# Kernel tuning notes

Hardware: AMD Instinct MI355X
Metric: run time of the kernel (lower is better)

## Reference

```python
import jax, jax.numpy as jnp
import numpy as np

HID = 2048
NH = 16
HD = HID // NH  # 128
SEQ = 2048
BSZ = 2
NEG = -1e9


def setup_inputs() -> dict:
    key = jax.random.key(0)
    ks = jax.random.split(key, 9)
    s = 0.02
    hidden_states = jax.random.normal(ks[0], (BSZ, SEQ, HID), jnp.float32)
    # additive causal mask [1,1,S,S]
    causal = jnp.tril(jnp.ones((SEQ, SEQ), jnp.bool_))
    attention_mask = jnp.where(causal, 0.0, NEG).astype(jnp.float32)[None, None]
    Wq = jax.random.normal(ks[1], (HID, NH * HD), jnp.float32) * s
    bq = jax.random.normal(ks[2], (NH * HD,), jnp.float32) * s
    Wk = jax.random.normal(ks[3], (HID, NH * HD), jnp.float32) * s
    bk = jax.random.normal(ks[4], (NH * HD,), jnp.float32) * s
    Wv = jax.random.normal(ks[5], (HID, NH * HD), jnp.float32) * s
    bv = jax.random.normal(ks[6], (NH * HD,), jnp.float32) * s
    Wo = jax.random.normal(ks[7], (NH * HD, HID), jnp.float32) * s
    return {"hidden_states": hidden_states, "attention_mask": attention_mask,
            "Wq": Wq, "bq": bq, "Wk": Wk, "bk": bk, "Wv": Wv, "bv": bv, "Wo": Wo}


def reference(hidden_states, attention_mask, Wq, bq, Wk, bk, Wv, bv, Wo):
    b, s, _ = hidden_states.shape
    # projections -> [b, h, s, d]
    q = (hidden_states @ Wq + bq).reshape(b, s, NH, HD).transpose(0, 2, 1, 3)
    k = (hidden_states @ Wk + bk).reshape(b, s, NH, HD).transpose(0, 2, 1, 3)
    v = (hidden_states @ Wv + bv).reshape(b, s, NH, HD).transpose(0, 2, 1, 3)
    # eager attention, materializing [b,h,s,s] scores as in the original
    scores = jnp.einsum('bhqd,bhkd->bhqk', q, k) / jnp.sqrt(jnp.float32(HD))
    scores = scores + attention_mask
    probs = jax.nn.softmax(scores.astype(jnp.float32), axis=-1).astype(q.dtype)
    ctx = jnp.einsum('bhqk,bhkd->bhqd', probs, v)
    ctx = ctx.transpose(0, 2, 1, 3).reshape(b, s, NH * HD)
    return ctx @ Wo
```

## Files before the change

### kernel.cpp

```cpp
#include <hip/hip_runtime.h>

#define SEQ 2048
#define HIDDEN 2048
#define NHEAD 16
#define HDIM 128
#define BSZ 2

typedef __attribute__((ext_vector_type(8))) short bf16x8;
typedef __attribute__((ext_vector_type(4))) float f32x4;
typedef __attribute__((ext_vector_type(16))) float f32x16;
typedef unsigned short u16;
typedef unsigned int u32;

__device__ __forceinline__ u16 f2bf(float f) {
  union { float f; u32 u; } v; v.f = f;
  u32 r = v.u + 0x7FFF + ((v.u >> 16) & 1);
  return (u16)(r >> 16);
}

__device__ __forceinline__ void gload_lds16(const void* g, void* l) {
  __builtin_amdgcn_global_load_lds((const __attribute__((address_space(1))) u32*)g,
                                   (__attribute__((address_space(3))) u32*)l, 16, 0, 0);
}

__device__ __forceinline__ u32 pkbf(float lo, float hi_) {
  u32 r;
  asm("v_cvt_pk_bf16_f32 %0, %1, %2" : "=v"(r) : "v"(lo), "v"(hi_));
  return r;
}

__device__ __forceinline__ void pl32swap(u32& a, u32& b) {
  asm("v_permlane32_swap_b32 %0, %1" : "+v"(a), "+v"(b));
}

__global__ void conv_hs_kernel(const float4* __restrict__ in, uint4* __restrict__ out) {
  int i = blockIdx.x * 256 + threadIdx.x;
  float4 a = in[2 * i], b = in[2 * i + 1];
  uint4 o;
  o.x = (u32)f2bf(a.x) | ((u32)f2bf(a.y) << 16);
  o.y = (u32)f2bf(a.z) | ((u32)f2bf(a.w) << 16);
  o.z = (u32)f2bf(b.x) | ((u32)f2bf(b.y) << 16);
  o.w = (u32)f2bf(b.z) | ((u32)f2bf(b.w) << 16);
  out[i] = o;
}

__global__ void transw_kernel(const float* __restrict__ W0, const float* __restrict__ W1,
                              const float* __restrict__ W2, const float* __restrict__ W3,
                              u16* __restrict__ T0, u16* __restrict__ T1,
                              u16* __restrict__ T2, u16* __restrict__ T3) {
  __shared__ float tile[32][33];
  const float* W; u16* T;
  switch (blockIdx.z) {
    case 0: W = W0; T = T0; break;
    case 1: W = W1; T = T1; break;
    case 2: W = W2; T = T2; break;
    default: W = W3; T = T3; break;
  }
  int n0 = blockIdx.x * 32, k0 = blockIdx.y * 32;
  int tx = threadIdx.x, ty = threadIdx.y;
  #pragma unroll
  for (int r = ty; r < 32; r += 8) tile[r][tx] = W[(k0 + r) * HIDDEN + n0 + tx];
  __syncthreads();
  #pragma unroll
  for (int r = ty; r < 32; r += 8) T[(n0 + r) * HIDDEN + k0 + tx] = f2bf(tile[tx][r]);
}

__device__ __forceinline__ void stageA8(const u16* Ag, u16* Al, int kt, int h, int tid) {
  const int c = tid;
  const int row = h * 64 + (c >> 3);
  const int slot = (c & 7) ^ (row & 7);
  gload_lds16(Ag + (size_t)row * HIDDEN + kt * 64 + slot * 8,
              (char*)Al + h * 8192 + c * 16);
}
__device__ __forceinline__ void stageB8(const u16* Bg, u16* Bl, int kt, int h, int tid) {
  #pragma unroll
  for (int i = 0; i < 2; i++) {
    const int c = tid + i * 512;
    const int row = h * 128 + (c >> 3);
    const int slot = (c & 7) ^ (row & 7);
    gload_lds16(Bg + (size_t)row * HIDDEN + kt * 64 + slot * 8,
                (char*)Bl + h * 16384 + c * 16);
  }
}

#define LDA8(dst, QA, mi, ks) { \
  const int row_ = (QA) * 64 + wr * 32 + (mi) * 16 + l15; \
  dst = *(const bf16x8*)((const char*)Acur + row_ * 128 + ((((ks) * 4 + l4) ^ (row_ & 7)) * 16)); }
#define LDB8(dst, QB, ni, ks) { \
  const int row_ = (QB) * 128 + wc * 32 + (ni) * 16 + l15; \
  dst = *(const bf16x8*)((const char*)Bcur + row_ * 128 + ((((ks) * 4 + l4) ^ (row_ & 7)) * 16)); }

#define MFMA_(a, b, c) __builtin_amdgcn_mfma_f32_16x16x32_bf16(a, b, c, 0, 0, 0)

#define PHASE8(QA, QB, STG, VM) { \
  bf16x8 a00, a10, a01, a11, b00, b10, b01, b11; \
  LDA8(a00, QA, 0, 0) LDA8(a10, QA, 1, 0) LDA8(a01, QA, 0, 1) LDA8(a11, QA, 1, 1) \
  LDB8(b00, QB, 0, 0) LDB8(b10, QB, 1, 0) LDB8(b01, QB, 0, 1) LDB8(b11, QB, 1, 1) \
  STG; \
  __builtin_amdgcn_s_barrier(); \
  __builtin_amdgcn_s_setprio(1); \
  acc[QA][QB][0][0] = MFMA_(a00, b00, acc[QA][QB][0][0]); \
  acc[QA][QB][0][1] = MFMA_(a00, b10, acc[QA][QB][0][1]); \
  acc[QA][QB][1][0] = MFMA_(a10, b00, acc[QA][QB][1][0]); \
  acc[QA][QB][1][1] = MFMA_(a10, b10, acc[QA][QB][1][1]); \
  acc[QA][QB][0][0] = MFMA_(a01, b01, acc[QA][QB][0][0]); \
  acc[QA][QB][0][1] = MFMA_(a01, b11, acc[QA][QB][0][1]); \
  acc[QA][QB][1][0] = MFMA_(a11, b01, acc[QA][QB][1][0]); \
  acc[QA][QB][1][1] = MFMA_(a11, b11, acc[QA][QB][1][1]); \
  __builtin_amdgcn_s_setprio(0); \
  asm volatile("s_waitcnt vmcnt(" VM ")" ::: "memory"); \
  __builtin_amdgcn_sched_barrier(0); \
  __builtin_amdgcn_s_barrier(); }

#define GEMM8_CORE(Ag, Bg) \
  __shared__ u16 AL[2][128 * 64]; \
  __shared__ u16 BL[2][256 * 64]; \
  const int tid = threadIdx.x, lane = tid & 63, w = tid >> 6; \
  const int wr = w >> 2, wc = w & 3, l15 = lane & 15, l4 = (lane >> 4) & 3; \
  f32x4 acc[2][2][2][2] = {}; \
  stageA8(Ag, AL[0], 0, 0, tid); \
  __builtin_amdgcn_sched_barrier(0); \
  stageB8(Bg, BL[0], 0, 0, tid); \
  __builtin_amdgcn_sched_barrier(0); \
  stageB8(Bg, BL[0], 0, 1, tid); \
  __builtin_amdgcn_sched_barrier(0); \
  stageA8(Ag, AL[0], 0, 1, tid); \
  asm volatile("s_waitcnt vmcnt(3)" ::: "memory"); \
  __builtin_amdgcn_sched_barrier(0); \
  __builtin_amdgcn_s_barrier(); \
  for (int t = 0; t < HIDDEN / 64; t++) { \
    const int cb = t & 1; \
    const u16* Acur = AL[cb]; const u16* Bcur = BL[cb]; \
    u16* An = AL[cb ^ 1]; u16* Bn = BL[cb ^ 1]; \
    const int kn = (t < HIDDEN / 64 - 1) ? t + 1 : t;   \
    PHASE8(0, 0, stageA8(Ag, An, kn, 0, tid), "2") \
    PHASE8(0, 1, stageB8(Bg, Bn, kn, 0, tid), "3") \
    PHASE8(1, 0, stageB8(Bg, Bn, kn, 1, tid), "5") \
    PHASE8(1, 1, stageA8(Ag, An, kn, 1, tid), "3") \
  }

__global__ __launch_bounds__(512, 1)
void qkv_gemm8(const u16* __restrict__ hsb, const u16* __restrict__ wT,
               const float* __restrict__ bq, const float* __restrict__ bk,
               const float* __restrict__ bv,
               u16* __restrict__ Qb, u16* __restrict__ Kb, u16* __restrict__ Vb) {
  const int o = blockIdx.x;
  const int wg = (o & 7) * 96 + (o >> 3);
  const int by = wg / 24, bx = wg % 24;
  const int z = bx >> 3;
  const u16* Ag = hsb + (size_t)by * 128 * HIDDEN;
  const u16* Bg = wT + (size_t)bx * 256 * HIDDEN;
  u16* dst = (z == 0) ? Qb : (z == 1) ? Kb : Vb;
  const float* bias = (z == 0) ? bq : (z == 1) ? bk : bv;
  const float scale = (z == 0) ? 0.08838834764831845f * 1.4426950408889634f : 1.0f;

  GEMM8_CORE(Ag, Bg)

  #pragma unroll
  for (int qa = 0; qa < 2; qa++)
    #pragma unroll
    for (int qb = 0; qb < 2; qb++)
      #pragma unroll
      for (int ni = 0; ni < 2; ni++) {
        const int n = bx * 256 + qb * 128 + wc * 32 + ni * 16 + l15;
        const int h_ = (n >> 7) & 15, d_ = n & 127;
        const float bv_ = bias[n & 2047];
        #pragma unroll
        for (int mi = 0; mi < 2; mi++)
          #pragma unroll
          for (int r = 0; r < 4; r++) {
            const int m = by * 128 + qa * 64 + wr * 32 + mi * 16 + l4 * 4 + r;
            const int b_ = m >> 11, s_ = m & 2047;
            dst[(((size_t)(b_ * NHEAD + h_) * SEQ) + s_) * HDIM + d_] =
                f2bf((acc[qa][qb][mi][ni][r] + bv_) * scale);
          }
      }
}

__global__ __launch_bounds__(512, 1)
void out_gemm8(const u16* __restrict__ ctxb, const u16* __restrict__ woT,
               float* __restrict__ out) {
  const int o = blockIdx.x;
  const int wg = (o & 7) * 32 + (o >> 3);
  const int by = wg >> 3, bx = wg & 7;
  const u16* Ag = ctxb + (size_t)by * 128 * HIDDEN;
  const u16* Bg = woT + (size_t)bx * 256 * HIDDEN;

  GEMM8_CORE(Ag, Bg)

  #pragma unroll
  for (int qa = 0; qa < 2; qa++)
    #pragma unroll
    for (int qb = 0; qb < 2; qb++)
      #pragma unroll
      for (int ni = 0; ni < 2; ni++) {
        const int n = bx * 256 + qb * 128 + wc * 32 + ni * 16 + l15;
        #pragma unroll
        for (int mi = 0; mi < 2; mi++)
          #pragma unroll
          for (int r = 0; r < 4; r++) {
            const int m = by * 128 + qa * 64 + wr * 32 + mi * 16 + l4 * 4 + r;
            out[(size_t)m * HIDDEN + n] = acc[qa][qb][mi][ni][r];
          }
      }
}

__global__ void transv_kernel(const u16* __restrict__ V, u16* __restrict__ VT) {
  __shared__ u16 tile[32][33];
  int bh = blockIdx.z;
  int d0 = blockIdx.x * 32, s0 = blockIdx.y * 32;
  const u16* Vp = V + (size_t)bh * SEQ * HDIM;
  u16* Tp = VT + (size_t)bh * HDIM * SEQ;
  int tx = threadIdx.x, ty = threadIdx.y;
  #pragma unroll
  for (int r = ty; r < 32; r += 8) tile[r][tx] = Vp[(s0 + r) * HDIM + d0 + tx];
  __syncthreads();
  #pragma unroll
  for (int r = ty; r < 32; r += 8) Tp[(d0 + r) * SEQ + s0 + tx] = tile[tx][r];
}

__device__ __forceinline__ void stage_tiles(u16* KLb, u16* VLb,
                                            const u16* Kg0, const u16* Vg0,
                                            int j, int w, int lane) {
  const u16* Kg = Kg0 + j * (64 * HDIM);
  const u16* Vg = Vg0 + j * 64;
  #pragma unroll
  for (int i = 0; i < 4; i++) {
    const int c = (w * 4 + i) * 64 + lane;
    const int row = c >> 4;
    const int inb = ((c & 15) * 16) ^ ((row & 7) << 4);
    gload_lds16(Kg + row * HDIM + (inb >> 1), (char*)KLb + c * 16);
  }
  #pragma unroll
  for (int i = 0; i < 4; i++) {
    const int c = (w * 4 + i) * 64 + lane;
    const int row = c >> 3;
    const int inb = ((c & 7) * 16) ^ ((row & 7) << 4);
    gload_lds16(Vg + row * SEQ + (inb >> 1), (char*)VLb + c * 16);
  }
}

__global__ __launch_bounds__(256)
void attn_kernel(const u16* __restrict__ Qb, const u16* __restrict__ Kb,
                 const u16* __restrict__ VbT, u16* __restrict__ ctx) {
  __shared__ u16 KL[2][64 * 128];
  __shared__ u16 VL[2][128 * 64];

  const int n = blockIdx.x;
  const int xcd = n & 7, slot = n >> 3;
  const int bh = xcd * 4 + (slot >> 3);
  const int xp = slot & 7;
  const int b = bh >> 4, h = bh & 15;
  const int tid = threadIdx.x, lane = tid & 63, w = tid >> 6;
  const int l31 = lane & 31, hi = lane >> 5;

  const u16* Kg0 = Kb + (size_t)bh * SEQ * HDIM;
  const u16* Vg0 = VbT + (size_t)bh * HDIM * SEQ;
  const u16* Qg0 = Qb + (size_t)bh * SEQ * HDIM;

  for (int ph = 0; ph < 2; ph++) {
    const int qt = ph ? (15 - xp) : xp;
    const int NT = 2 * qt + 2;
    const int q0w = qt * 128 + w * 32;
    const int qlane = q0w + l31;

    bf16x8 qf[8];
    #pragma unroll
    for (int c = 0; c < 8; c++)
      qf[c] = *(const bf16x8*)(Qg0 + (size_t)qlane * HDIM + c * 16 + hi * 8);

    f32x16 o0 = {}, o1 = {}, o2 = {}, o3 = {};
    float m_run = -1e30f, l_run = 0.0f;

    int cb = 0;
    stage_tiles(&KL[0][0], &VL[0][0], Kg0, Vg0, 0, w, lane);
    __syncthreads();

    for (int j = 0; j < NT; j++) {
      if (j + 1 < NT)
        stage_tiles(&KL[cb ^ 1][0], &VL[cb ^ 1][0], Kg0, Vg0, j + 1, w, lane);

      f32x16 s0 = {}, s1 = {};
      #pragma unroll
      for (int c = 0; c < 8; c++) {
        const int cbyte = c * 32 + hi * 16;
        const int r0 = l31, r1 = 32 + l31;
        bf16x8 k0 = *(const bf16x8*)((const char*)&KL[cb][0] + (r0 * 256 + (cbyte ^ ((r0 & 7) << 4))));
        bf16x8 k1 = *(const bf16x8*)((const char*)&KL[cb][0] + (r1 * 256 + (cbyte ^ ((r1 & 7) << 4))));
        s0 = __builtin_amdgcn_mfma_f32_32x32x16_bf16(k0, qf[c], s0, 0, 0, 0);
        s1 = __builtin_amdgcn_mfma_f32_32x32x16_bf16(k1, qf[c], s1, 0, 0, 0);
      }

      if (j >= NT - 2) {
        const int kvb = j * 64 + 4 * hi;
        #pragma unroll
        for (int r = 0; r < 16; r++) {
          const int kr = kvb + (r & 3) + 8 * (r >> 2);
          if (kr > qlane) s0[r] = -1e9f;
          if (kr + 32 > qlane) s1[r] = -1e9f;
        }
      }

      float pm = s0[0];
      #pragma unroll
      for (int r = 1; r < 16; r++) pm = fmaxf(pm, s0[r]);
      #pragma unroll
      for (int r = 0; r < 16; r++) pm = fmaxf(pm, s1[r]);
      pm = fmaxf(pm, __shfl_xor(pm, 32));

      if (!__all(pm - m_run <= 8.0f)) {
        const float mn = fmaxf(m_run, pm);
        const float al = exp2f(m_run - mn);
        l_run *= al;
        #pragma unroll
        for (int r = 0; r < 16; r++) {
          const float ar = __shfl(al, (r & 3) + 8 * (r >> 2) + 4 * hi);
          o0[r] *= ar; o1[r] *= ar; o2[r] *= ar; o3[r] *= ar;
        }
        m_run = mn;
      }

      float rs = 0.0f;
      #pragma unroll
      for (int r = 0; r < 16; r++) { s0[r] = exp2f(s0[r] - m_run); rs += s0[r]; }
      #pragma unroll
      for (int r = 0; r < 16; r++) { s1[r] = exp2f(s1[r] - m_run); rs += s1[r]; }
      rs += __shfl_xor(rs, 32);
      l_run += rs;

      union { u32 wd[4]; bf16x8 v; } pa0, pa1, pa2, pa3;
      { u32 A0 = pkbf(s0[0], s0[1]),  B0 = pkbf(s0[4], s0[5]);  pl32swap(A0, B0);
        u32 A1 = pkbf(s0[2], s0[3]),  B1 = pkbf(s0[6], s0[7]);  pl32swap(A1, B1);
        pa0.wd[0] = A0; pa0.wd[1] = A1; pa0.wd[2] = B0; pa0.wd[3] = B1; }
      { u32 A0 = pkbf(s0[8], s0[9]),  B0 = pkbf(s0[12], s0[13]); pl32swap(A0, B0);
        u32 A1 = pkbf(s0[10], s0[11]), B1 = pkbf(s0[14], s0[15]); pl32swap(A1, B1);
        pa1.wd[0] = A0; pa1.wd[1] = A1; pa1.wd[2] = B0; pa1.wd[3] = B1; }
      { u32 A0 = pkbf(s1[0], s1[1]),  B0 = pkbf(s1[4], s1[5]);  pl32swap(A0, B0);
        u32 A1 = pkbf(s1[2], s1[3]),  B1 = pkbf(s1[6], s1[7]);  pl32swap(A1, B1);
        pa2.wd[0] = A0; pa2.wd[1] = A1; pa2.wd[2] = B0; pa2.wd[3] = B1; }
      { u32 A0 = pkbf(s1[8], s1[9]),  B0 = pkbf(s1[12], s1[13]); pl32swap(A0, B0);
        u32 A1 = pkbf(s1[10], s1[11]), B1 = pkbf(s1[14], s1[15]); pl32swap(A1, B1);
        pa3.wd[0] = A0; pa3.wd[1] = A1; pa3.wd[2] = B0; pa3.wd[3] = B1; }

#define PV_D(OD, DS) { \
      const int row = (DS) * 32 + l31; \
      const int sw = (row & 7) << 4; \
      const char* vbase = (const char*)&VL[cb][0] + row * 128; \
      bf16x8 v0 = *(const bf16x8*)(vbase + ((  0 + hi * 16) ^ sw)); \
      bf16x8 v1 = *(const bf16x8*)(vbase + (( 32 + hi * 16) ^ sw)); \
      bf16x8 v2 = *(const bf16x8*)(vbase + (( 64 + hi * 16) ^ sw)); \
      bf16x8 v3 = *(const bf16x8*)(vbase + (( 96 + hi * 16) ^ sw)); \
      OD = __builtin_amdgcn_mfma_f32_32x32x16_bf16(pa0.v, v0, OD, 0, 0, 0); \
      OD = __builtin_amdgcn_mfma_f32_32x32x16_bf16(pa1.v, v1, OD, 0, 0, 0); \
      OD = __builtin_amdgcn_mfma_f32_32x32x16_bf16(pa2.v, v2, OD, 0, 0, 0); \
      OD = __builtin_amdgcn_mfma_f32_32x32x16_bf16(pa3.v, v3, OD, 0, 0, 0); }
      PV_D(o0, 0) PV_D(o1, 1) PV_D(o2, 2) PV_D(o3, 3)
#undef PV_D

      __syncthreads();
      cb ^= 1;
    }

    const float invl = 1.0f / l_run;
    #pragma unroll
    for (int r = 0; r < 16; r++) {
      const int qr = (r & 3) + 8 * (r >> 2) + 4 * hi;
      const float iv = __shfl(invl, qr);
      const size_t base = ((size_t)b * SEQ + (q0w + qr)) * HIDDEN + h * HDIM + l31;
      ctx[base +  0] = f2bf(o0[r] * iv);
      ctx[base + 32] = f2bf(o1[r] * iv);
      ctx[base + 64] = f2bf(o2[r] * iv);
      ctx[base + 96] = f2bf(o3[r] * iv);
    }
  }
}

extern "C" void kernel_launch(void* const* d_in, const int* in_sizes, int n_in,
                              void* d_out, int out_size, void* d_ws, size_t ws_size,
                              hipStream_t stream) {
  const float* hs = (const float*)d_in[0];
  const float* Wq = (const float*)d_in[2];
  const float* bq = (const float*)d_in[3];
  const float* Wk = (const float*)d_in[4];
  const float* bk = (const float*)d_in[5];
  const float* Wv = (const float*)d_in[6];
  const float* bv = (const float*)d_in[7];
  const float* Wo = (const float*)d_in[8];
  float* out = (float*)d_out;

  char* ws = (char*)d_ws;
  const size_t MB = 1024 * 1024;
  u16* hsb = (u16*)(ws + 0);
  u16* wqT = (u16*)(ws + 16 * MB);
  u16* wkT = (u16*)(ws + 24 * MB);
  u16* wvT = (u16*)(ws + 32 * MB);
  u16* woT = (u16*)(ws + 40 * MB);
  u16* Qb  = (u16*)(ws + 48 * MB);
  u16* Kb  = (u16*)(ws + 64 * MB);
  u16* Vb  = (u16*)(ws + 80 * MB);
  u16* VbT = (u16*)(ws + 0);
  u16* ctx = (u16*)(ws + 16 * MB);

  conv_hs_kernel<<<4096, 256, 0, stream>>>((const float4*)hs, (uint4*)hsb);
  transw_kernel<<<dim3(64, 64, 4), dim3(32, 8), 0, stream>>>(Wq, Wk, Wv, Wo, wqT, wkT, wvT, woT);
  qkv_gemm8<<<768, 512, 0, stream>>>(hsb, wqT, bq, bk, bv, Qb, Kb, Vb);
  transv_kernel<<<dim3(4, 64, 32), dim3(32, 8), 0, stream>>>(Vb, VbT);
  attn_kernel<<<dim3(256), 256, 0, stream>>>(Qb, Kb, VbT, ctx);
  out_gemm8<<<256, 512, 0, stream>>>(ctx, woT, out);
  (void)in_sizes; (void)n_in; (void)out_size; (void)ws_size;
}
```

Before: 471.3 us.

## Use triple-buffered LDS pipeline with two-phase K-step in projection GEMMs

Replaces the double-buffered four-phase GEMM main loop with a three-stage LDS ring buffer that prefetches two K-tiles ahead. Each K-step now runs in two phases: all A fragments plus half of B are loaded and 16 MFMAs issued per phase, which halves the barriers per K-step and keeps A fragments in registers. This aims to hide global-load latency and cut barrier overhead, at the cost of 50% more LDS (limiting occupancy, already one block per CU) and more registers.

```diff
diff --git a/kernel.cpp b/kernel.cpp
--- a/kernel.cpp
+++ b/kernel.cpp
@@ -72,15 +72,12 @@
   gload_lds16(Ag + (size_t)row * HIDDEN + kt * 64 + slot * 8,
               (char*)Al + h * 8192 + c * 16);
 }
-__device__ __forceinline__ void stageB8(const u16* Bg, u16* Bl, int kt, int h, int tid) {
-  #pragma unroll
-  for (int i = 0; i < 2; i++) {
-    const int c = tid + i * 512;
-    const int row = h * 128 + (c >> 3);
-    const int slot = (c & 7) ^ (row & 7);
-    gload_lds16(Bg + (size_t)row * HIDDEN + kt * 64 + slot * 8,
-                (char*)Bl + h * 16384 + c * 16);
-  }
+__device__ __forceinline__ void stageBq(const u16* Bg, u16* Bl, int kt, int q, int tid) {
+  const int c = tid + q * 512;
+  const int row = c >> 3;
+  const int slot = (c & 7) ^ (row & 7);
+  gload_lds16(Bg + (size_t)row * HIDDEN + kt * 64 + slot * 8,
+              (char*)Bl + c * 16);
 }
 
 #define LDA8(dst, QA, mi, ks) { \
@@ -92,52 +89,62 @@
 
 #define MFMA_(a, b, c) __builtin_amdgcn_mfma_f32_16x16x32_bf16(a, b, c, 0, 0, 0)
 
-#define PHASE8(QA, QB, STG, VM) { \
-  bf16x8 a00, a10, a01, a11, b00, b10, b01, b11; \
-  LDA8(a00, QA, 0, 0) LDA8(a10, QA, 1, 0) LDA8(a01, QA, 0, 1) LDA8(a11, QA, 1, 1) \
-  LDB8(b00, QB, 0, 0) LDB8(b10, QB, 1, 0) LDB8(b01, QB, 0, 1) LDB8(b11, QB, 1, 1) \
-  STG; \
-  __builtin_amdgcn_s_barrier(); \
-  __builtin_amdgcn_s_setprio(1); \
-  acc[QA][QB][0][0] = MFMA_(a00, b00, acc[QA][QB][0][0]); \
-  acc[QA][QB][0][1] = MFMA_(a00, b10, acc[QA][QB][0][1]); \
-  acc[QA][QB][1][0] = MFMA_(a10, b00, acc[QA][QB][1][0]); \
-  acc[QA][QB][1][1] = MFMA_(a10, b10, acc[QA][QB][1][1]); \
-  acc[QA][QB][0][0] = MFMA_(a01, b01, acc[QA][QB][0][0]); \
-  acc[QA][QB][0][1] = MFMA_(a01, b11, acc[QA][QB][0][1]); \
-  acc[QA][QB][1][0] = MFMA_(a11, b01, acc[QA][QB][1][0]); \
-  acc[QA][QB][1][1] = MFMA_(a11, b11, acc[QA][QB][1][1]); \
-  __builtin_amdgcn_s_setprio(0); \
-  asm volatile("s_waitcnt vmcnt(" VM ")" ::: "memory"); \
-  __builtin_amdgcn_sched_barrier(0); \
-  __builtin_amdgcn_s_barrier(); }
-
-#define GEMM8_CORE(Ag, Bg) \
-  __shared__ u16 AL[2][128 * 64]; \
-  __shared__ u16 BL[2][256 * 64]; \
+#define QUAD(QA, QB, A00, A10, A01, A11) \
+  acc[QA][QB][0][0] = MFMA_(A00, b00, acc[QA][QB][0][0]); \
+  acc[QA][QB][0][1] = MFMA_(A00, b10, acc[QA][QB][0][1]); \
+  acc[QA][QB][1][0] = MFMA_(A10, b00, acc[QA][QB][1][0]); \
+  acc[QA][QB][1][1] = MFMA_(A10, b10, acc[QA][QB][1][1]); \
+  acc[QA][QB][0][0] = MFMA_(A01, b01, acc[QA][QB][0][0]); \
+  acc[QA][QB][0][1] = MFMA_(A01, b11, acc[QA][QB][0][1]); \
+  acc[QA][QB][1][0] = MFMA_(A11, b01, acc[QA][QB][1][0]); \
+  acc[QA][QB][1][1] = MFMA_(A11, b11, acc[QA][QB][1][1]);
+
+#define GEMM3_CORE(Ag, Bg) \
+  __shared__ u16 AL[3][128 * 64]; \
+  __shared__ u16 BL[3][256 * 64]; \
   const int tid = threadIdx.x, lane = tid & 63, w = tid >> 6; \
   const int wr = w >> 2, wc = w & 3, l15 = lane & 15, l4 = (lane >> 4) & 3; \
   f32x4 acc[2][2][2][2] = {}; \
-  stageA8(Ag, AL[0], 0, 0, tid); \
-  __builtin_amdgcn_sched_barrier(0); \
-  stageB8(Bg, BL[0], 0, 0, tid); \
-  __builtin_amdgcn_sched_barrier(0); \
-  stageB8(Bg, BL[0], 0, 1, tid); \
-  __builtin_amdgcn_sched_barrier(0); \
-  stageA8(Ag, AL[0], 0, 1, tid); \
-  asm volatile("s_waitcnt vmcnt(3)" ::: "memory"); \
+  stageA8(Ag, AL[0], 0, 0, tid); stageA8(Ag, AL[0], 0, 1, tid); \
+  stageBq(Bg, BL[0], 0, 0, tid); stageBq(Bg, BL[0], 0, 1, tid); \
+  stageBq(Bg, BL[0], 0, 2, tid); stageBq(Bg, BL[0], 0, 3, tid); \
+  stageA8(Ag, AL[1], 1, 0, tid); stageA8(Ag, AL[1], 1, 1, tid); \
+  stageBq(Bg, BL[1], 1, 0, tid); stageBq(Bg, BL[1], 1, 1, tid); \
+  stageBq(Bg, BL[1], 1, 2, tid); stageBq(Bg, BL[1], 1, 3, tid); \
+  asm volatile("s_waitcnt vmcnt(8)" ::: "memory"); \
   __builtin_amdgcn_sched_barrier(0); \
   __builtin_amdgcn_s_barrier(); \
-  for (int t = 0; t < HIDDEN / 64; t++) { \
-    const int cb = t & 1; \
-    const u16* Acur = AL[cb]; const u16* Bcur = BL[cb]; \
-    u16* An = AL[cb ^ 1]; u16* Bn = BL[cb ^ 1]; \
-    const int kn = (t < HIDDEN / 64 - 1) ? t + 1 : t;   \
-    PHASE8(0, 0, stageA8(Ag, An, kn, 0, tid), "2") \
-    PHASE8(0, 1, stageB8(Bg, Bn, kn, 0, tid), "3") \
-    PHASE8(1, 0, stageB8(Bg, Bn, kn, 1, tid), "5") \
-    PHASE8(1, 1, stageA8(Ag, An, kn, 1, tid), "3") \
-  }
+  int curb = 0, stgb = 2; \
+  for (int t = 0; t < 32; t++) { \
+    const u16* Acur = AL[curb]; const u16* Bcur = BL[curb]; \
+    u16* An = AL[stgb]; u16* Bn = BL[stgb]; \
+    const int kn = (t + 2 < 32) ? t + 2 : 31;   \
+    bf16x8 a000, a010, a001, a011, a100, a110, a101, a111, b00, b10, b01, b11; \
+    LDA8(a000, 0, 0, 0) LDA8(a010, 0, 1, 0) LDA8(a001, 0, 0, 1) LDA8(a011, 0, 1, 1) \
+    LDA8(a100, 1, 0, 0) LDA8(a110, 1, 1, 0) LDA8(a101, 1, 0, 1) LDA8(a111, 1, 1, 1) \
+    LDB8(b00, 0, 0, 0) LDB8(b10, 0, 1, 0) LDB8(b01, 0, 0, 1) LDB8(b11, 0, 1, 1) \
+    stageA8(Ag, An, kn, 0, tid); stageA8(Ag, An, kn, 1, tid); \
+    stageBq(Bg, Bn, kn, 0, tid); \
+    __builtin_amdgcn_s_setprio(1); \
+    QUAD(0, 0, a000, a010, a001, a011) \
+    QUAD(1, 0, a100, a110, a101, a111) \
+    __builtin_amdgcn_s_setprio(0); \
+    asm volatile("s_waitcnt vmcnt(9)" ::: "memory"); \
+    __builtin_amdgcn_sched_barrier(0); \
+    __builtin_amdgcn_s_barrier(); \
+    LDB8(b00, 1, 0, 0) LDB8(b10, 1, 1, 0) LDB8(b01, 1, 0, 1) LDB8(b11, 1, 1, 1) \
+    stageBq(Bg, Bn, kn, 1, tid); stageBq(Bg, Bn, kn, 2, tid); stageBq(Bg, Bn, kn, 3, tid); \
+    __builtin_amdgcn_s_setprio(1); \
+    QUAD(0, 1, a000, a010, a001, a011) \
+    QUAD(1, 1, a100, a110, a101, a111) \
+    __builtin_amdgcn_s_setprio(0); \
+    asm volatile("s_waitcnt vmcnt(8)" ::: "memory"); \
+    __builtin_amdgcn_sched_barrier(0); \
+    __builtin_amdgcn_s_barrier(); \
+    curb = (curb == 2) ? 0 : curb + 1; \
+    stgb = (stgb == 2) ? 0 : stgb + 1; \
+  } \
+  asm volatile("s_waitcnt vmcnt(0)" ::: "memory");
 
 __global__ __launch_bounds__(512, 1)
 void qkv_gemm8(const u16* __restrict__ hsb, const u16* __restrict__ wT,
@@ -154,7 +161,7 @@
   const float* bias = (z == 0) ? bq : (z == 1) ? bk : bv;
   const float scale = (z == 0) ? 0.08838834764831845f * 1.4426950408889634f : 1.0f;
 
-  GEMM8_CORE(Ag, Bg)
+  GEMM3_CORE(Ag, Bg)
 
   #pragma unroll
   for (int qa = 0; qa < 2; qa++)
@@ -186,7 +193,7 @@
   const u16* Ag = ctxb + (size_t)by * 128 * HIDDEN;
   const u16* Bg = woT + (size_t)bx * 256 * HIDDEN;
 
-  GEMM8_CORE(Ag, Bg)
+  GEMM3_CORE(Ag, Bg)
 
   #pragma unroll
   for (int qa = 0; qa < 2; qa++)
```

Measured after the change: 401.3 us. 1.17x faster.
